# Performance work log

Measured on AMD Instinct MI355X. Metric: run time of the kernel, lower is better.

## Reference

```python
import jax, jax.numpy as jnp
import numpy as np

Nc, Nq = 100000, 20000
Fc, Fq = 300, 768
HID, H, L = 128, 4, 2
D = HID // H
OUT = 8
E = 400000
NT, ET = 2, 3


def setup_inputs() -> dict:
    key = jax.random.key(0)
    ks = jax.random.split(key, 24)
    def n(i, shape, s=1.0):
        return jax.random.normal(ks[i], shape, dtype=jnp.float32) * s
    return {
        'x_context': n(0, (Nc, Fc)),
        'x_question': n(1, (Nq, Fq)),
        'src_q2c': jax.random.randint(ks[2], (E,), 0, Nq),
        'dst_q2c': jax.random.randint(ks[3], (E,), 0, Nc),
        'src_c2c': jax.random.randint(ks[4], (E,), 0, Nc),
        'dst_c2c': jax.random.randint(ks[5], (E,), 0, Nc),
        'src_c2q': jax.random.randint(ks[6], (E,), 0, Nc),
        'dst_c2q': jax.random.randint(ks[7], (E,), 0, Nq),
        'in_W_context': n(8, (Fc, HID), 0.05),
        'in_b_context': jnp.zeros((HID,), jnp.float32),
        'in_W_question': n(9, (Fq, HID), 0.05),
        'in_b_question': jnp.zeros((HID,), jnp.float32),
        'k_W': n(10, (L, NT, HID, HID), 0.05),
        'k_b': jnp.zeros((L, NT, HID), jnp.float32),
        'q_W': n(11, (L, NT, HID, HID), 0.05),
        'q_b': jnp.zeros((L, NT, HID), jnp.float32),
        'v_W': n(12, (L, NT, HID, HID), 0.05),
        'v_b': jnp.zeros((L, NT, HID), jnp.float32),
        'a_W': n(13, (L, NT, HID, HID), 0.05),
        'a_b': jnp.zeros((L, NT, HID), jnp.float32),
        'skip': jnp.ones((L, NT), jnp.float32),
        'a_rel': n(14, (L, ET, H, D, D), 0.1),
        'm_rel': n(15, (L, ET, H, D, D), 0.1),
        'p_rel': jnp.ones((L, ET, H), jnp.float32),
        'out_W': n(16, (HID, OUT), 0.05),
        'out_b': jnp.zeros((OUT,), jnp.float32),
    }


def segment_softmax(logits, seg, num):
    # logits: [E, H], seg: [E] destination node ids
    m = jax.ops.segment_max(logits, seg, num_segments=num)
    m = jnp.where(jnp.isfinite(m), m, 0.0)
    e = jnp.exp(logits - m[seg])
    s = jax.ops.segment_sum(e, seg, num_segments=num)
    return e / (s[seg] + 1e-16)


def reference(x_context, x_question, src_q2c, dst_q2c, src_c2c, dst_c2c,
              src_c2q, dst_c2q, in_W_context, in_b_context, in_W_question,
              in_b_question, k_W, k_b, q_W, q_b, v_W, v_b, a_W, a_b, skip,
              a_rel, m_rel, p_rel, out_W, out_b):
    # node type 0 = 'context', 1 = 'question'
    x = [jax.nn.relu(x_context @ in_W_context + in_b_context),
         jax.nn.relu(x_question @ in_W_question + in_b_question)]
    Ns = [x[0].shape[0], x[1].shape[0]]
    # (src_nt, dst_nt, src_idx, dst_idx) per edge type
    edge_types = [(1, 0, src_q2c, dst_q2c),
                  (0, 0, src_c2c, dst_c2c),
                  (0, 1, src_c2q, dst_c2q)]
    scale = 1.0 / jnp.sqrt(jnp.float32(D))
    for l in range(L):
        k = [(x[nt] @ k_W[l, nt] + k_b[l, nt]).reshape(-1, H, D) for nt in range(NT)]
        q = [(x[nt] @ q_W[l, nt] + q_b[l, nt]).reshape(-1, H, D) for nt in range(NT)]
        v = [(x[nt] @ v_W[l, nt] + v_b[l, nt]).reshape(-1, H, D) for nt in range(NT)]
        agg = [jnp.zeros((Ns[nt], H, D), x[0].dtype) for nt in range(NT)]
        for et, (snt, dnt, src, dst) in enumerate(edge_types):
            k_rel = jnp.einsum('ehd,hdf->ehf', k[snt][src], a_rel[l, et])
            v_rel = jnp.einsum('ehd,hdf->ehf', v[snt][src], m_rel[l, et])
            logits = jnp.einsum('ehd,ehd->eh', q[dnt][dst], k_rel) * p_rel[l, et] * scale
            alpha = segment_softmax(logits, dst, Ns[dnt])  # [E, H]
            agg[dnt] = agg[dnt].at[dst].add(v_rel * alpha[:, :, None])
        for nt in range(NT):
            o = jax.nn.gelu(agg[nt].reshape(Ns[nt], HID), approximate=False)
            o = o @ a_W[l, nt] + a_b[l, nt]
            g = jax.nn.sigmoid(skip[l, nt])
            x[nt] = g * o + (1.0 - g) * x[nt]
    return x[0] @ out_W + out_b
```

## Files before the change

kernel.cpp:

```cpp
#include <hip/hip_runtime.h>

constexpr int NC = 100000;
constexpr int NQ = 20000;
constexpr int FC = 300;
constexpr int FQ = 768;
constexpr int NEDGE = 400000;
constexpr int NTOT = NC + NC + NQ;
constexpr int NTOT2 = NC + NQ;
constexpr int NB0 = (NC + 127) / 128;
constexpr int NB1 = (NQ + 127) / 128;
constexpr int NBALL = NB0 + NB1;
constexpr int NBC64 = (NC + 63) / 64;
constexpr int NBQ64 = (NQ + 63) / 64;
constexpr int NBALL64 = NBC64 + NBQ64;
constexpr float SCALE = 0.17677669529663687f;
constexpr float LOG2E = 1.4426950408889634f;

typedef __attribute__((ext_vector_type(8))) short bf16x8;
typedef __attribute__((ext_vector_type(4))) float f32x4;
typedef unsigned short u16;

__device__ __forceinline__ float gelu_f(float x) {
  return 0.5f * x * (1.0f + erff(x * 0.7071067811865476f));
}
__device__ __forceinline__ u16 bf16_rne(float x) {
  unsigned u = __float_as_uint(x);
  unsigned r = u + 0x7fffu + ((u >> 16) & 1u);
  return (u16)(r >> 16);
}
__device__ __forceinline__ float bf16_to_f(u16 h) {
  return __uint_as_float(((unsigned)h) << 16);
}
__device__ __forceinline__ void split2(float x, u16& hi, u16& lo) {
  hi = bf16_rne(x);
  lo = bf16_rne(x - bf16_to_f(hi));
}
__device__ __forceinline__ void splitT(float x, u16& hi, u16& lo) {
  hi = (u16)(__float_as_uint(x) >> 16);
  lo = bf16_rne(x - bf16_to_f(hi));
}

__global__ void k_count3(const int* __restrict__ d0, const int* __restrict__ d1,
                         const int* __restrict__ d2, int* __restrict__ counts) {
  int i = blockIdx.x * 256 + threadIdx.x;
  if (i >= 3 * NEDGE) return;
  int et = i / NEDGE, e = i - et * NEDGE;
  int d = (et == 0) ? d0[e] : (et == 1) ? d1[e] : d2[e];
  int base = (et == 0) ? 0 : (et == 1) ? NC : 2 * NC;
  atomicAdd(&counts[base + d], 1);
}

__global__ void k_scan_block(const int* __restrict__ in, int* __restrict__ out,
                             int* __restrict__ bsum, int n) {
  __shared__ int s[256];
  int tid = threadIdx.x;
  int i = blockIdx.x * 256 + tid;
  int v = (i < n) ? in[i] : 0;
  s[tid] = v;
  __syncthreads();
  for (int off = 1; off < 256; off <<= 1) {
    int t = (tid >= off) ? s[tid - off] : 0;
    __syncthreads();
    s[tid] += t;
    __syncthreads();
  }
  if (i < n) out[i] = s[tid] - v;
  if (tid == 255) bsum[blockIdx.x] = s[255];
}

__global__ void k_scan_sums(int* __restrict__ bsum, int nb) {
  __shared__ int s[1024];
  int tid = threadIdx.x;
  int v = (tid < nb) ? bsum[tid] : 0;
  s[tid] = v;
  __syncthreads();
  for (int off = 1; off < 1024; off <<= 1) {
    int t = (tid >= off) ? s[tid - off] : 0;
    __syncthreads();
    s[tid] += t;
    __syncthreads();
  }
  if (tid < nb) bsum[tid] = s[tid] - v;
}

__global__ void k_scan_add(int* __restrict__ ptr, const int* __restrict__ bsum,
                           int* __restrict__ cursor, int n, int total) {
  int i = blockIdx.x * 256 + threadIdx.x;
  if (i < n) {
    int v = ptr[i] + bsum[blockIdx.x];
    ptr[i] = v;
    cursor[i] = v;
  }
  if (i == 0) ptr[n] = total;
}

__global__ void k_scatter3(const int* __restrict__ s0, const int* __restrict__ s1,
                           const int* __restrict__ s2, const int* __restrict__ d0,
                           const int* __restrict__ d1, const int* __restrict__ d2,
                           int* __restrict__ cursor, int* __restrict__ srcs_out) {
  int i = blockIdx.x * 256 + threadIdx.x;
  if (i >= 3 * NEDGE) return;
  int et = i / NEDGE, e = i - et * NEDGE;
  int d = (et == 0) ? d0[e] : (et == 1) ? d1[e] : d2[e];
  int sv = (et == 0) ? s0[e] : (et == 1) ? s1[e] : s2[e];
  int base = (et == 0) ? 0 : (et == 1) ? NC : 2 * NC;
  int p = atomicAdd(&cursor[base + d], 1);
  srcs_out[p] = sv;
}

__global__ void prep_all(const float* __restrict__ kW, const float* __restrict__ kB,
                         const float* __restrict__ qW, const float* __restrict__ qB,
                         const float* __restrict__ vW, const float* __restrict__ vB,
                         const float* __restrict__ aW, const float* __restrict__ aB,
                         const float* __restrict__ arel, const float* __restrict__ mrel,
                         const float* __restrict__ prel,
                         u16* __restrict__ Bth, u16* __restrict__ Btl,
                         float* __restrict__ biasOut) {
  int i = blockIdx.x;
  int col = threadIdx.x;
  int y = blockIdx.y;
  int l = y / 10, yy = y % 10;
  size_t lw = (size_t)l * 2 * 16384, lb = (size_t)l * 2 * 128;
  size_t le = (size_t)l * 3 * 4096, lp = (size_t)l * 3 * 4;
  const float *W = nullptr, *bb = nullptr, *rel = nullptr, *pr = nullptr;
  float mscale = 1.0f;
  bool fold = false;
  switch (yy) {
    case 0: W = qW + lw; bb = qB + lb; break;
    case 1: fold = true; W = kW + lw; bb = kB + lb; rel = arel + le + 4096; pr = prel + lp + 4; mscale = SCALE; break;
    case 2: fold = true; W = vW + lw; bb = vB + lb; rel = mrel + le + 4096; break;
    case 3: fold = true; W = kW + lw; bb = kB + lb; rel = arel + le + 8192; pr = prel + lp + 8; mscale = SCALE; break;
    case 4: fold = true; W = vW + lw; bb = vB + lb; rel = mrel + le + 8192; break;
    case 5: W = qW + lw + 16384; bb = qB + lb + 128; break;
    case 6: fold = true; W = kW + lw + 16384; bb = kB + lb + 128; rel = arel + le; pr = prel + lp; mscale = SCALE; break;
    case 7: fold = true; W = vW + lw + 16384; bb = vB + lb + 128; rel = mrel + le; break;
    case 8: W = aW + lw; bb = aB + lb; break;
    default: W = aW + lw + 16384; bb = aB + lb + 128; break;
  }
  int colOff = y * 128;
  if (!fold) {
    float v = W[i * 128 + col];
    u16 hi, lo;
    split2(v, hi, lo);
    Bth[(size_t)(colOff + col) * 128 + i] = hi;
    Btl[(size_t)(colOff + col) * 128 + i] = lo;
    if (i == 0) biasOut[colOff + col] = bb[col];
    return;
  }
  int h = col >> 5, f = col & 31;
  float m = (pr ? pr[h] : 1.0f) * mscale;
  float s = 0.0f;
  #pragma unroll
  for (int d = 0; d < 32; ++d)
    s += W[i * 128 + h * 32 + d] * rel[(h * 32 + d) * 32 + f];
  s *= m;
  u16 hi, lo;
  split2(s, hi, lo);
  Bth[(size_t)(colOff + col) * 128 + i] = hi;
  Btl[(size_t)(colOff + col) * 128 + i] = lo;
  if (i == 0) {
    float sb = 0.0f;
    #pragma unroll
    for (int d = 0; d < 32; ++d)
      sb += bb[h * 32 + d] * rel[(h * 32 + d) * 32 + f];
    biasOut[colOff + col] = sb * m;
  }
}

__global__ void split_in(const float* __restrict__ Wc, const float* __restrict__ bc,
                         const float* __restrict__ Wq, const float* __restrict__ bq,
                         u16* __restrict__ Bth, u16* __restrict__ Btl,
                         float* __restrict__ biasOut) {
  int n = blockIdx.x, y = blockIdx.y;
  const float* W = y ? Wq : Wc;
  const float* b = y ? bq : bc;
  int K = y ? FQ : FC, Kp = y ? 768 : 320;
  size_t boff = y ? (size_t)128 * 320 : 0;
  for (int k = threadIdx.x; k < Kp; k += 256) {
    float v = (k < K) ? W[(size_t)k * 128 + n] : 0.0f;
    u16 hi, lo;
    split2(v, hi, lo);
    Bth[boff + (size_t)n * Kp + k] = hi;
    Btl[boff + (size_t)n * Kp + k] = lo;
  }
  if (threadIdx.x == 0) biasOut[(y ? 128 : 0) + n] = b[n];
}

template <int MODE>
__global__ __launch_bounds__(256) void pipe_gemm(
    const float* __restrict__ Ac, const float* __restrict__ Aq,
    const u16* __restrict__ Bth, const u16* __restrict__ Btl,
    const float* __restrict__ biasBuf,
    u16* __restrict__ xh_all, u16* __restrict__ xl_all,
    const float* __restrict__ skip, int l) {
  __shared__ u16 smem[15360];
  constexpr int AH = 0, AL = 2560, BH = 5120, BL = 10240;
  const int tid = threadIdx.x, lane = tid & 63, wv = tid >> 6;
  const int l15 = lane & 15, g4 = lane >> 4, koff = g4 * 8;
  const int srA = tid >> 2, scA = (tid & 3) * 8;
  const int srB = tid >> 1, scB = (tid & 1) * 16;

  const int bid = blockIdx.x;
  const int nt = (bid < NBC64) ? 0 : 1;
  const int m0 = nt ? (bid - NBC64) * 64 : bid * 64;
  const int M = nt ? NQ : NC;
  const int rowbase = nt ? NC : 0;
  const float* A32;
  int K, Kp, biasOff;
  size_t boff, arow;
  if (MODE == 1) {
    if (nt == 0) { A32 = Ac; K = FC; Kp = 320; boff = 0; biasOff = 0; }
    else { A32 = Aq; K = FQ; Kp = 768; boff = (size_t)128 * 320; biasOff = 128; }
    arow = (size_t)(m0 + srA) * K;
  } else {
    A32 = Ac;
    K = 128; Kp = 128;
    boff = (size_t)(8 + nt) * 16384;
    biasOff = (8 + nt) * 128;
    arow = (size_t)(rowbase + m0 + srA) * 128;
  }
  const bool rowokA = (m0 + srA) < M;
  const int nk = (K + 31) / 32;

  f32x4 acc[8];
  #pragma unroll
  for (int ni = 0; ni < 8; ++ni) acc[ni] = (f32x4){0.f, 0.f, 0.f, 0.f};

  auto loadA = [&](float va[8], int k0) {
    if (rowokA && (k0 + 32 <= K)) {
      const float* ap = A32 + arow + k0 + scA;
      float4 f0 = *(const float4*)ap;
      float4 f1 = *(const float4*)(ap + 4);
      va[0] = f0.x; va[1] = f0.y; va[2] = f0.z; va[3] = f0.w;
      va[4] = f1.x; va[5] = f1.y; va[6] = f1.z; va[7] = f1.w;
    } else {
      #pragma unroll
      for (int j = 0; j < 8; ++j) {
        int kc = k0 + scA + j;
        va[j] = (rowokA && kc < K) ? A32[arow + kc] : 0.0f;
      }
    }
  };
  auto loadB = [&](uint4& bh0, uint4& bh1, uint4& bl0, uint4& bl1, int k0) {
    const u16* bp = Bth + boff + (size_t)srB * Kp + k0 + scB;
    bh0 = *(const uint4*)bp;
    bh1 = *(const uint4*)(bp + 8);
    const u16* lp = Btl + boff + (size_t)srB * Kp + k0 + scB;
    bl0 = *(const uint4*)lp;
    bl1 = *(const uint4*)(lp + 8);
  };

  float vaC[8];
  uint4 bhC0, bhC1, blC0, blC1;
  loadA(vaC, 0);
  loadB(bhC0, bhC1, blC0, blC1, 0);

  for (int ks = 0; ks < nk; ++ks) {
    {
      alignas(16) u16 hv[8], lv[8];
      #pragma unroll
      for (int j = 0; j < 8; ++j) {
        float x = (MODE == 2) ? gelu_f(vaC[j]) : vaC[j];
        splitT(x, hv[j], lv[j]);
      }
      *(uint4*)&smem[AH + srA * 40 + scA] = *(const uint4*)hv;
      *(uint4*)&smem[AL + srA * 40 + scA] = *(const uint4*)lv;
      *(uint4*)&smem[BH + srB * 40 + scB] = bhC0;
      *(uint4*)&smem[BH + srB * 40 + scB + 8] = bhC1;
      *(uint4*)&smem[BL + srB * 40 + scB] = blC0;
      *(uint4*)&smem[BL + srB * 40 + scB + 8] = blC1;
    }
    __syncthreads();

    float vaN[8];
    uint4 bhN0, bhN1, blN0, blN1;
    const bool more = (ks + 1) < nk;
    if (more) {
      loadA(vaN, (ks + 1) * 32);
      loadB(bhN0, bhN1, blN0, blN1, (ks + 1) * 32);
    }

    {
      int row = wv * 16 + l15;
      bf16x8 a_h = *(const bf16x8*)&smem[AH + row * 40 + koff];
      bf16x8 a_l = *(const bf16x8*)&smem[AL + row * 40 + koff];
      #pragma unroll
      for (int ni = 0; ni < 8; ++ni) {
        int col = ni * 16 + l15;
        bf16x8 b_h = *(const bf16x8*)&smem[BH + col * 40 + koff];
        bf16x8 b_l = *(const bf16x8*)&smem[BL + col * 40 + koff];
        acc[ni] = __builtin_amdgcn_mfma_f32_16x16x32_bf16(a_h, b_h, acc[ni], 0, 0, 0);
        acc[ni] = __builtin_amdgcn_mfma_f32_16x16x32_bf16(a_l, b_h, acc[ni], 0, 0, 0);
        acc[ni] = __builtin_amdgcn_mfma_f32_16x16x32_bf16(a_h, b_l, acc[ni], 0, 0, 0);
      }
    }
    __syncthreads();

    if (more) {
      #pragma unroll
      for (int j = 0; j < 8; ++j) vaC[j] = vaN[j];
      bhC0 = bhN0; bhC1 = bhN1; blC0 = blN0; blC1 = blN1;
    }
  }

  float g = 1.0f;
  if (MODE == 2) g = 1.0f / (1.0f + __expf(-skip[l * 2 + nt]));

  const int rl0 = wv * 16 + g4 * 4;
  #pragma unroll
  for (int ni = 0; ni < 8; ++ni) {
    int colL = ni * 16 + l15;
    float bi = biasBuf[biasOff + colL];
    #pragma unroll
    for (int rr = 0; rr < 4; ++rr) {
      int row = m0 + rl0 + rr;
      float o = acc[ni][rr] + bi;
      if (MODE == 1) {
        o = fmaxf(o, 0.0f);
      } else if (row < M) {
        size_t idx = (size_t)(rowbase + row) * 128 + colL;
        float xo = bf16_to_f(xh_all[idx]) + bf16_to_f(xl_all[idx]);
        o = g * o + (1.0f - g) * xo;
      }
      acc[ni][rr] = o;
    }
  }

  const int wrow = tid >> 2, wseg = tid & 3;
  #pragma unroll
  for (int ph = 0; ph < 2; ++ph) {
    if (ph) __syncthreads();
    #pragma unroll
    for (int ni = 0; ni < 8; ++ni) {
      #pragma unroll
      for (int rr = 0; rr < 4; ++rr) {
        u16 hh, ll;
        split2(acc[ni][rr], hh, ll);
        smem[(rl0 + rr) * 136 + ni * 16 + l15] = ph ? ll : hh;
      }
    }
    __syncthreads();
    int grow = m0 + wrow;
    if (grow < M) {
      u16* dstp = ph ? xl_all : xh_all;
      uint4* dst = (uint4*)&dstp[(size_t)(rowbase + grow) * 128 + wseg * 32];
      const uint4* src = (const uint4*)&smem[wrow * 136 + wseg * 32];
      #pragma unroll
      for (int j = 0; j < 4; ++j) dst[j] = src[j];
    }
  }
}

__global__ __launch_bounds__(256) void proj_all(
    const u16* __restrict__ xh_all,
    const u16* __restrict__ Bth, const float* __restrict__ biasBuf,
    u16* __restrict__ q_all, u16* __restrict__ kvA,
    u16* __restrict__ kvB1, u16* __restrict__ kvB2, int last) {
  int bid = blockIdx.x, y = blockIdx.y;
  int nt = (bid < NB0) ? 0 : 1;
  if (nt == 1 && y >= 3) return;
  if (last) {
    if (nt == 0 && y >= 3) return;
    if (nt == 1 && y == 0) return;
  }
  __shared__ u16 smem[10240];
  constexpr int AH = 0, BH = 5120;
  int m0 = nt ? (bid - NB0) * 128 : bid * 128;
  int M = nt ? NQ : NC;
  int abase = nt ? NC : 0;
  int bslab = nt ? 5 + y : y;
  u16* cp; int ld, cb, crowbase;
  if (nt == 0) {
    switch (y) {
      case 0: cp = q_all; ld = 128; cb = 0; crowbase = 0; break;
      case 1: cp = kvB1; ld = 256; cb = 0; crowbase = 0; break;
      case 2: cp = kvB1; ld = 256; cb = 128; crowbase = 0; break;
      case 3: cp = kvB2; ld = 256; cb = 0; crowbase = 0; break;
      default: cp = kvB2; ld = 256; cb = 128; crowbase = 0; break;
    }
  } else {
    switch (y) {
      case 0: cp = q_all; ld = 128; cb = 0; crowbase = NC; break;
      case 1: cp = kvA; ld = 256; cb = 0; crowbase = 0; break;
      default: cp = kvA; ld = 256; cb = 128; crowbase = 0; break;
    }
  }
  const int tid = threadIdx.x, lane = tid & 63, wv = tid >> 6;
  const int l15 = lane & 15, g4 = lane >> 4, koff = g4 * 8;
  const int sr = tid >> 1, sc = (tid & 1) * 16;
  const bool rowok = (m0 + sr) < M;

  f32x4 acc[2][8];
  #pragma unroll
  for (int mi = 0; mi < 2; ++mi)
    #pragma unroll
    for (int ni = 0; ni < 8; ++ni) acc[mi][ni] = (f32x4){0.f, 0.f, 0.f, 0.f};

  for (int k0 = 0; k0 < 128; k0 += 32) {
    uint4 h0 = {0, 0, 0, 0}, h1 = {0, 0, 0, 0};
    if (rowok) {
      const u16* ap = xh_all + (size_t)(abase + m0 + sr) * 128 + k0 + sc;
      h0 = *(const uint4*)ap;
      h1 = *(const uint4*)(ap + 8);
    }
    *(uint4*)&smem[AH + sr * 40 + sc] = h0;
    *(uint4*)&smem[AH + sr * 40 + sc + 8] = h1;
    {
      const u16* bp = Bth + (size_t)(bslab * 128 + sr) * 128 + k0 + sc;
      *(uint4*)&smem[BH + sr * 40 + sc] = *(const uint4*)bp;
      *(uint4*)&smem[BH + sr * 40 + sc + 8] = *(const uint4*)(bp + 8);
    }
    __syncthreads();

    bf16x8 a_h[2];
    #pragma unroll
    for (int mi = 0; mi < 2; ++mi) {
      int row = wv * 32 + mi * 16 + l15;
      a_h[mi] = *(const bf16x8*)&smem[AH + row * 40 + koff];
    }
    #pragma unroll
    for (int ni = 0; ni < 8; ++ni) {
      int col = ni * 16 + l15;
      bf16x8 b_h = *(const bf16x8*)&smem[BH + col * 40 + koff];
      #pragma unroll
      for (int mi = 0; mi < 2; ++mi)
        acc[mi][ni] = __builtin_amdgcn_mfma_f32_16x16x32_bf16(a_h[mi], b_h, acc[mi][ni], 0, 0, 0);
    }
    __syncthreads();
  }

  const int wrow = tid >> 2, wseg = tid & 3;
  #pragma unroll
  for (int h = 0; h < 2; ++h) {
    if (h) __syncthreads();
    if ((wv >> 1) == h) {
      #pragma unroll
      for (int mi = 0; mi < 2; ++mi) {
        int rl = (wv & 1) * 32 + mi * 16 + g4 * 4;
        #pragma unroll
        for (int ni = 0; ni < 8; ++ni) {
          float bi = biasBuf[bslab * 128 + ni * 16 + l15];
          #pragma unroll
          for (int rr = 0; rr < 4; ++rr)
            smem[(rl + rr) * 136 + ni * 16 + l15] = bf16_rne(acc[mi][ni][rr] + bi);
        }
      }
    }
    __syncthreads();
    int grow = m0 + h * 64 + wrow;
    if (grow < M) {
      uint4* dst = (uint4*)&cp[(size_t)(crowbase + grow) * ld + cb + wseg * 32];
      const uint4* src = (const uint4*)&smem[wrow * 136 + wseg * 32];
      #pragma unroll
      for (int j = 0; j < 4; ++j) dst[j] = src[j];
    }
  }
}

__device__ __forceinline__ void attn_seg(
    const u16* __restrict__ kv, int start, int end,
    const int* __restrict__ srcs, const float q8[8], int lane, float accO[8]) {
  if (start >= end) return;
  float sum = 0.0f;
  float acc[8];
  #pragma unroll
  for (int i = 0; i < 8; ++i) acc[i] = 0.0f;
  const int half = lane >> 5;
  const int sub = lane & 31;
  const int bsrc = lane & 44;
  for (int e = start; e < end; e += 4) {
    int e0 = e + half;
    int e1 = e + 2 + half;
    bool v0 = e0 < end, v1 = e1 < end;
    int c0 = v0 ? e0 : end - 1;
    int c1 = v1 ? e1 : end - 1;
    int s0 = srcs[c0];
    int s1 = srcs[c1];
    uint4 u0 = *(const uint4*)&kv[(size_t)s0 * 256 + sub * 8];
    uint4 u1 = *(const uint4*)&kv[(size_t)s1 * 256 + sub * 8];
    float r0[8], r1[8];
    r0[0] = bf16_to_f((u16)(u0.x & 0xffffu)); r0[1] = bf16_to_f((u16)(u0.x >> 16));
    r0[2] = bf16_to_f((u16)(u0.y & 0xffffu)); r0[3] = bf16_to_f((u16)(u0.y >> 16));
    r0[4] = bf16_to_f((u16)(u0.z & 0xffffu)); r0[5] = bf16_to_f((u16)(u0.z >> 16));
    r0[6] = bf16_to_f((u16)(u0.w & 0xffffu)); r0[7] = bf16_to_f((u16)(u0.w >> 16));
    r1[0] = bf16_to_f((u16)(u1.x & 0xffffu)); r1[1] = bf16_to_f((u16)(u1.x >> 16));
    r1[2] = bf16_to_f((u16)(u1.y & 0xffffu)); r1[3] = bf16_to_f((u16)(u1.y >> 16));
    r1[4] = bf16_to_f((u16)(u1.z & 0xffffu)); r1[5] = bf16_to_f((u16)(u1.z >> 16));
    r1[6] = bf16_to_f((u16)(u1.w & 0xffffu)); r1[7] = bf16_to_f((u16)(u1.w >> 16));
    float p0 = q8[0] * r0[0];
    float p1 = q8[0] * r1[0];
    #pragma unroll
    for (int i = 1; i < 8; ++i) {
      p0 = fmaf(q8[i], r0[i], p0);
      p1 = fmaf(q8[i], r1[i], p1);
    }
    p0 += __shfl_xor(p0, 1);
    p1 += __shfl_xor(p1, 1);
    p0 += __shfl_xor(p0, 2);
    p1 += __shfl_xor(p1, 2);
    p0 = fminf(p0, 100.0f);
    p1 = fminf(p1, 100.0f);
    float w0 = v0 ? exp2f(p0) : 0.0f;
    float w1 = v1 ? exp2f(p1) : 0.0f;
    float wB0 = __shfl(w0, bsrc);
    float wB1 = __shfl(w1, bsrc);
    sum += wB0 + wB1;
    #pragma unroll
    for (int i = 0; i < 8; ++i) {
      acc[i] = fmaf(wB0, r0[i], acc[i]);
      acc[i] = fmaf(wB1, r1[i], acc[i]);
    }
  }
  sum += __shfl_xor(sum, 32);
  #pragma unroll
  for (int i = 0; i < 8; ++i) acc[i] += __shfl_xor(acc[i], 32);
  float inv = 1.0f / (sum + 1e-16f);
  #pragma unroll
  for (int i = 0; i < 8; ++i) accO[i] = fmaf(acc[i], inv, accO[i]);
}

__global__ __launch_bounds__(256) void attn_all(
    const u16* __restrict__ q_all, const u16* __restrict__ kvA,
    const u16* __restrict__ kvB1, const u16* __restrict__ kvB2,
    const int* __restrict__ ptr_all, const int* __restrict__ srcs_all,
    float* __restrict__ agg_all, int ncap) {
  int wave = threadIdx.x >> 6, lane = threadIdx.x & 63;
  int node = blockIdx.x * 4 + wave;
  if (node >= ncap) return;
  int sub = lane & 31;
  float q8[8];
  #pragma unroll
  for (int i = 0; i < 8; ++i) q8[i] = 0.0f;
  if (sub < 16) {
    uint4 u = *(const uint4*)&q_all[(size_t)node * 128 + sub * 8];
    q8[0] = bf16_to_f((u16)(u.x & 0xffffu)) * LOG2E; q8[1] = bf16_to_f((u16)(u.x >> 16)) * LOG2E;
    q8[2] = bf16_to_f((u16)(u.y & 0xffffu)) * LOG2E; q8[3] = bf16_to_f((u16)(u.y >> 16)) * LOG2E;
    q8[4] = bf16_to_f((u16)(u.z & 0xffffu)) * LOG2E; q8[5] = bf16_to_f((u16)(u.z >> 16)) * LOG2E;
    q8[6] = bf16_to_f((u16)(u.w & 0xffffu)) * LOG2E; q8[7] = bf16_to_f((u16)(u.w >> 16)) * LOG2E;
  }
  float accO[8];
  #pragma unroll
  for (int i = 0; i < 8; ++i) accO[i] = 0.0f;
  if (node < NC) {
    attn_seg(kvA, ptr_all[node], ptr_all[node + 1], srcs_all, q8, lane, accO);
    attn_seg(kvB1, ptr_all[NC + node], ptr_all[NC + node + 1], srcs_all, q8, lane, accO);
  } else {
    int idx = 2 * NC + (node - NC);
    attn_seg(kvB2, ptr_all[idx], ptr_all[idx + 1], srcs_all, q8, lane, accO);
  }
  if (lane >= 16 && lane < 32) {
    int j = lane - 16;
    float4 o0 = {accO[0], accO[1], accO[2], accO[3]};
    float4 o1 = {accO[4], accO[5], accO[6], accO[7]};
    *(float4*)&agg_all[(size_t)node * 128 + j * 8] = o0;
    *(float4*)&agg_all[(size_t)node * 128 + j * 8 + 4] = o1;
  }
}

__global__ __launch_bounds__(256) void gemm_out(const u16* __restrict__ Xh,
                                                const u16* __restrict__ Xl,
                                                const float* __restrict__ W,
                                                const float* __restrict__ b,
                                                float* __restrict__ out, int M) {
  __shared__ float Ws[1024];
  __shared__ float As[32][129];
  int tid = threadIdx.x;
  int m0 = blockIdx.x * 32;
  *(float4*)&Ws[tid * 4] = *(const float4*)&W[tid * 4];
  {
    int r = tid >> 3;
    int c0 = (tid & 7) * 16;
    if (m0 + r < M) {
      const u16* hp = Xh + (size_t)(m0 + r) * 128 + c0;
      const u16* lp = Xl + (size_t)(m0 + r) * 128 + c0;
      #pragma unroll
      for (int j = 0; j < 16; ++j) As[r][c0 + j] = bf16_to_f(hp[j]) + bf16_to_f(lp[j]);
    } else {
      #pragma unroll
      for (int j = 0; j < 16; ++j) As[r][c0 + j] = 0.0f;
    }
  }
  __syncthreads();
  int r = tid >> 3, c = tid & 7;
  float sum = b[c];
  #pragma unroll 16
  for (int k = 0; k < 128; ++k) sum = fmaf(As[r][k], Ws[k * 8 + c], sum);
  if (m0 + r < M) out[(size_t)(m0 + r) * 8 + c] = sum;
}

static inline size_t align256(size_t x) { return (x + 255) & ~(size_t)255; }

extern "C" void kernel_launch(void* const* d_in, const int* in_sizes, int n_in,
                              void* d_out, int out_size, void* d_ws, size_t ws_size,
                              hipStream_t stream) {
  const float* x_context = (const float*)d_in[0];
  const float* x_question = (const float*)d_in[1];
  const int* src_q2c = (const int*)d_in[2];
  const int* dst_q2c = (const int*)d_in[3];
  const int* src_c2c = (const int*)d_in[4];
  const int* dst_c2c = (const int*)d_in[5];
  const int* src_c2q = (const int*)d_in[6];
  const int* dst_c2q = (const int*)d_in[7];
  const float* inWc = (const float*)d_in[8];
  const float* inbc = (const float*)d_in[9];
  const float* inWq = (const float*)d_in[10];
  const float* inbq = (const float*)d_in[11];
  const float* kW = (const float*)d_in[12];
  const float* kB = (const float*)d_in[13];
  const float* qW = (const float*)d_in[14];
  const float* qB = (const float*)d_in[15];
  const float* vW = (const float*)d_in[16];
  const float* vB = (const float*)d_in[17];
  const float* aW = (const float*)d_in[18];
  const float* aB = (const float*)d_in[19];
  const float* skip = (const float*)d_in[20];
  const float* arel = (const float*)d_in[21];
  const float* mrel = (const float*)d_in[22];
  const float* prel = (const float*)d_in[23];
  const float* outW = (const float*)d_in[24];
  const float* outb = (const float*)d_in[25];

  char* base = (char*)d_ws;
  size_t off = 0;
  auto carve = [&](size_t bytes) -> void* {
    void* p = base + off;
    off = align256(off + bytes);
    return p;
  };
  u16* xh_all = (u16*)carve((size_t)NTOT2 * 128 * 2);
  u16* xl_all = (u16*)carve((size_t)NTOT2 * 128 * 2);
  u16* q_all = (u16*)carve((size_t)NTOT2 * 128 * 2);
  u16* kvA = (u16*)carve((size_t)NQ * 256 * 2);
  u16* kvB1 = (u16*)carve((size_t)NC * 256 * 2);
  u16* kvB2 = (u16*)carve((size_t)NC * 256 * 2);
  float* agg_all = (float*)carve((size_t)NTOT2 * 128 * 4);
  u16* Bth = (u16*)carve((size_t)2560 * 128 * 2);
  u16* Btl = (u16*)carve((size_t)2560 * 128 * 2);
  u16* BthI = (u16*)carve((size_t)(320 + 768) * 128 * 2);
  u16* BtlI = (u16*)carve((size_t)(320 + 768) * 128 * 2);
  float* biasBuf = (float*)carve(2560 * 4);
  float* biasIn = (float*)carve(256 * 4);
  int* ptr_all = (int*)carve((size_t)(NTOT + 1) * 4);
  int* srcs_all = (int*)carve((size_t)3 * NEDGE * 4);
  int* counts = (int*)carve((size_t)NTOT * 4);
  int* cursor = (int*)carve((size_t)NTOT * 4);
  int* blksums = (int*)carve(2048 * 4);

  {
    int nb = (NTOT + 255) / 256;
    hipMemsetAsync(counts, 0, (size_t)NTOT * 4, stream);
    k_count3<<<(3 * NEDGE + 255) / 256, 256, 0, stream>>>(dst_q2c, dst_c2c, dst_c2q, counts);
    k_scan_block<<<nb, 256, 0, stream>>>(counts, ptr_all, blksums, NTOT);
    k_scan_sums<<<1, 1024, 0, stream>>>(blksums, nb);
    k_scan_add<<<nb, 256, 0, stream>>>(ptr_all, blksums, cursor, NTOT, 3 * NEDGE);
    k_scatter3<<<(3 * NEDGE + 255) / 256, 256, 0, stream>>>(
        src_q2c, src_c2c, src_c2q, dst_q2c, dst_c2c, dst_c2q, cursor, srcs_all);
  }

  split_in<<<dim3(128, 2), 256, 0, stream>>>(inWc, inbc, inWq, inbq, BthI, BtlI, biasIn);
  prep_all<<<dim3(128, 20), 128, 0, stream>>>(kW, kB, qW, qB, vW, vB, aW, aB,
                                              arel, mrel, prel, Bth, Btl, biasBuf);

  pipe_gemm<1><<<NBALL64, 256, 0, stream>>>(x_context, x_question, BthI, BtlI, biasIn,
                                            xh_all, xl_all, nullptr, 0);

  for (int l = 0; l < 2; ++l) {
    const int last = (l == 1);
    const u16* BthL = Bth + (size_t)l * 10 * 128 * 128;
    const u16* BtlL = Btl + (size_t)l * 10 * 128 * 128;
    const float* biasL = biasBuf + (size_t)l * 1280;
    proj_all<<<dim3(NBALL, 5), 256, 0, stream>>>(xh_all, BthL, biasL,
                                                 q_all, kvA, kvB1, kvB2, last);
    int ncap = last ? NC : NTOT2;
    attn_all<<<(ncap + 3) / 4, 256, 0, stream>>>(q_all, kvA, kvB1, kvB2,
                                                 ptr_all, srcs_all, agg_all, ncap);
    pipe_gemm<2><<<last ? NBC64 : NBALL64, 256, 0, stream>>>(agg_all, nullptr, BthL, BtlL, biasL,
                                                             xh_all, xl_all, skip, l);
  }

  gemm_out<<<(NC + 31) / 32, 256, 0, stream>>>(xh_all, xl_all, outW, outb, (float*)d_out, NC);
}
```

Measured before the change: 696.2 us.

## Use 128-row tiles in input and output GEMMs, drop prefetch and A-low split for GELU path

The input-projection and post-attention GEMMs now use 128-row tiles with two M sub-tiles per wave instead of 64-row tiles, so each B fragment loaded from LDS feeds twice as many MFMAs. The register prefetch of the next K slice is removed, leaving a plain load-sync-compute loop. In the GELU (MODE 2) path the activation is rounded to a single bf16 instead of a hi/lo pair, which drops one of the three MFMAs per fragment at some precision cost. The epilogue writes out the 128-row tile in two halves through shared memory.

```diff
diff --git a/kernel.cpp b/kernel.cpp
--- a/kernel.cpp
+++ b/kernel.cpp
@@ -10,9 +10,6 @@
 constexpr int NB0 = (NC + 127) / 128;
 constexpr int NB1 = (NQ + 127) / 128;
 constexpr int NBALL = NB0 + NB1;
-constexpr int NBC64 = (NC + 63) / 64;
-constexpr int NBQ64 = (NQ + 63) / 64;
-constexpr int NBALL64 = NBC64 + NBQ64;
 constexpr float SCALE = 0.17677669529663687f;
 constexpr float LOG2E = 1.4426950408889634f;
 
@@ -187,22 +184,25 @@
 }
 
 template <int MODE>
-__global__ __launch_bounds__(256) void pipe_gemm(
+__global__ __launch_bounds__(256) void big_gemm(
     const float* __restrict__ Ac, const float* __restrict__ Aq,
     const u16* __restrict__ Bth, const u16* __restrict__ Btl,
     const float* __restrict__ biasBuf,
     u16* __restrict__ xh_all, u16* __restrict__ xl_all,
     const float* __restrict__ skip, int l) {
-  __shared__ u16 smem[15360];
-  constexpr int AH = 0, AL = 2560, BH = 5120, BL = 10240;
+  constexpr int NS = (MODE == 1) ? 20480 : 15360;
+  constexpr int AHo = 0;
+  constexpr int ALo = 5120;
+  constexpr int BHo = (MODE == 1) ? 10240 : 5120;
+  constexpr int BLo = BHo + 5120;
+  __shared__ u16 smem[NS];
   const int tid = threadIdx.x, lane = tid & 63, wv = tid >> 6;
   const int l15 = lane & 15, g4 = lane >> 4, koff = g4 * 8;
-  const int srA = tid >> 2, scA = (tid & 3) * 8;
-  const int srB = tid >> 1, scB = (tid & 1) * 16;
+  const int sr = tid >> 1, sc16 = (tid & 1) * 16;
 
   const int bid = blockIdx.x;
-  const int nt = (bid < NBC64) ? 0 : 1;
-  const int m0 = nt ? (bid - NBC64) * 64 : bid * 64;
+  const int nt = (bid < NB0) ? 0 : 1;
+  const int m0 = nt ? (bid - NB0) * 128 : bid * 128;
   const int M = nt ? NQ : NC;
   const int rowbase = nt ? NC : 0;
   const float* A32;
@@ -211,142 +211,141 @@
   if (MODE == 1) {
     if (nt == 0) { A32 = Ac; K = FC; Kp = 320; boff = 0; biasOff = 0; }
     else { A32 = Aq; K = FQ; Kp = 768; boff = (size_t)128 * 320; biasOff = 128; }
-    arow = (size_t)(m0 + srA) * K;
+    arow = (size_t)(m0 + sr) * K;
   } else {
     A32 = Ac;
     K = 128; Kp = 128;
     boff = (size_t)(8 + nt) * 16384;
     biasOff = (8 + nt) * 128;
-    arow = (size_t)(rowbase + m0 + srA) * 128;
-  }
-  const bool rowokA = (m0 + srA) < M;
-  const int nk = (K + 31) / 32;
-
-  f32x4 acc[8];
-  #pragma unroll
-  for (int ni = 0; ni < 8; ++ni) acc[ni] = (f32x4){0.f, 0.f, 0.f, 0.f};
-
-  auto loadA = [&](float va[8], int k0) {
+    arow = (size_t)(rowbase + m0 + sr) * 128;
+  }
+  const bool rowokA = (m0 + sr) < M;
+
+  f32x4 acc[2][8];
+  #pragma unroll
+  for (int mi = 0; mi < 2; ++mi)
+    #pragma unroll
+    for (int ni = 0; ni < 8; ++ni) acc[mi][ni] = (f32x4){0.f, 0.f, 0.f, 0.f};
+
+  for (int k0 = 0; k0 < K; k0 += 32) {
+    float va[16];
     if (rowokA && (k0 + 32 <= K)) {
-      const float* ap = A32 + arow + k0 + scA;
-      float4 f0 = *(const float4*)ap;
-      float4 f1 = *(const float4*)(ap + 4);
-      va[0] = f0.x; va[1] = f0.y; va[2] = f0.z; va[3] = f0.w;
-      va[4] = f1.x; va[5] = f1.y; va[6] = f1.z; va[7] = f1.w;
+      const float* ap = A32 + arow + k0 + sc16;
+      #pragma unroll
+      for (int j = 0; j < 4; ++j) {
+        float4 f = *(const float4*)(ap + 4 * j);
+        va[4 * j + 0] = f.x; va[4 * j + 1] = f.y; va[4 * j + 2] = f.z; va[4 * j + 3] = f.w;
+      }
     } else {
       #pragma unroll
-      for (int j = 0; j < 8; ++j) {
-        int kc = k0 + scA + j;
+      for (int j = 0; j < 16; ++j) {
+        int kc = k0 + sc16 + j;
         va[j] = (rowokA && kc < K) ? A32[arow + kc] : 0.0f;
       }
     }
-  };
-  auto loadB = [&](uint4& bh0, uint4& bh1, uint4& bl0, uint4& bl1, int k0) {
-    const u16* bp = Bth + boff + (size_t)srB * Kp + k0 + scB;
-    bh0 = *(const uint4*)bp;
-    bh1 = *(const uint4*)(bp + 8);
-    const u16* lp = Btl + boff + (size_t)srB * Kp + k0 + scB;
-    bl0 = *(const uint4*)lp;
-    bl1 = *(const uint4*)(lp + 8);
-  };
-
-  float vaC[8];
-  uint4 bhC0, bhC1, blC0, blC1;
-  loadA(vaC, 0);
-  loadB(bhC0, bhC1, blC0, blC1, 0);
-
-  for (int ks = 0; ks < nk; ++ks) {
+    if (MODE == 1) {
+      alignas(16) u16 hv[16], lv[16];
+      #pragma unroll
+      for (int j = 0; j < 16; ++j) splitT(va[j], hv[j], lv[j]);
+      *(uint4*)&smem[AHo + sr * 40 + sc16] = *(const uint4*)&hv[0];
+      *(uint4*)&smem[AHo + sr * 40 + sc16 + 8] = *(const uint4*)&hv[8];
+      *(uint4*)&smem[ALo + sr * 40 + sc16] = *(const uint4*)&lv[0];
+      *(uint4*)&smem[ALo + sr * 40 + sc16 + 8] = *(const uint4*)&lv[8];
+    } else {
+      alignas(16) u16 hv[16];
+      #pragma unroll
+      for (int j = 0; j < 16; ++j) hv[j] = bf16_rne(gelu_f(va[j]));
+      *(uint4*)&smem[AHo + sr * 40 + sc16] = *(const uint4*)&hv[0];
+      *(uint4*)&smem[AHo + sr * 40 + sc16 + 8] = *(const uint4*)&hv[8];
+    }
     {
-      alignas(16) u16 hv[8], lv[8];
-      #pragma unroll
-      for (int j = 0; j < 8; ++j) {
-        float x = (MODE == 2) ? gelu_f(vaC[j]) : vaC[j];
-        splitT(x, hv[j], lv[j]);
+      const u16* bp = Bth + boff + (size_t)sr * Kp + k0 + sc16;
+      *(uint4*)&smem[BHo + sr * 40 + sc16] = *(const uint4*)bp;
+      *(uint4*)&smem[BHo + sr * 40 + sc16 + 8] = *(const uint4*)(bp + 8);
+      const u16* lp = Btl + boff + (size_t)sr * Kp + k0 + sc16;
+      *(uint4*)&smem[BLo + sr * 40 + sc16] = *(const uint4*)lp;
+      *(uint4*)&smem[BLo + sr * 40 + sc16 + 8] = *(const uint4*)(lp + 8);
+    }
+    __syncthreads();
+
+    bf16x8 a_h[2], a_l[2];
+    #pragma unroll
+    for (int mi = 0; mi < 2; ++mi) {
+      int row = wv * 32 + mi * 16 + l15;
+      a_h[mi] = *(const bf16x8*)&smem[AHo + row * 40 + koff];
+      if (MODE == 1) a_l[mi] = *(const bf16x8*)&smem[ALo + row * 40 + koff];
+    }
+    #pragma unroll
+    for (int ni = 0; ni < 8; ++ni) {
+      int col = ni * 16 + l15;
+      bf16x8 b_h = *(const bf16x8*)&smem[BHo + col * 40 + koff];
+      bf16x8 b_l = *(const bf16x8*)&smem[BLo + col * 40 + koff];
+      #pragma unroll
+      for (int mi = 0; mi < 2; ++mi) {
+        acc[mi][ni] = __builtin_amdgcn_mfma_f32_16x16x32_bf16(a_h[mi], b_h, acc[mi][ni], 0, 0, 0);
+        if (MODE == 1)
+          acc[mi][ni] = __builtin_amdgcn_mfma_f32_16x16x32_bf16(a_l[mi], b_h, acc[mi][ni], 0, 0, 0);
+        acc[mi][ni] = __builtin_amdgcn_mfma_f32_16x16x32_bf16(a_h[mi], b_l, acc[mi][ni], 0, 0, 0);
       }
-      *(uint4*)&smem[AH + srA * 40 + scA] = *(const uint4*)hv;
-      *(uint4*)&smem[AL + srA * 40 + scA] = *(const uint4*)lv;
-      *(uint4*)&smem[BH + srB * 40 + scB] = bhC0;
-      *(uint4*)&smem[BH + srB * 40 + scB + 8] = bhC1;
-      *(uint4*)&smem[BL + srB * 40 + scB] = blC0;
-      *(uint4*)&smem[BL + srB * 40 + scB + 8] = blC1;
-    }
-    __syncthreads();
-
-    float vaN[8];
-    uint4 bhN0, bhN1, blN0, blN1;
-    const bool more = (ks + 1) < nk;
-    if (more) {
-      loadA(vaN, (ks + 1) * 32);
-      loadB(bhN0, bhN1, blN0, blN1, (ks + 1) * 32);
-    }
-
-    {
-      int row = wv * 16 + l15;
-      bf16x8 a_h = *(const bf16x8*)&smem[AH + row * 40 + koff];
-      bf16x8 a_l = *(const bf16x8*)&smem[AL + row * 40 + koff];
-      #pragma unroll
-      for (int ni = 0; ni < 8; ++ni) {
-        int col = ni * 16 + l15;
-        bf16x8 b_h = *(const bf16x8*)&smem[BH + col * 40 + koff];
-        bf16x8 b_l = *(const bf16x8*)&smem[BL + col * 40 + koff];
-        acc[ni] = __builtin_amdgcn_mfma_f32_16x16x32_bf16(a_h, b_h, acc[ni], 0, 0, 0);
-        acc[ni] = __builtin_amdgcn_mfma_f32_16x16x32_bf16(a_l, b_h, acc[ni], 0, 0, 0);
-        acc[ni] = __builtin_amdgcn_mfma_f32_16x16x32_bf16(a_h, b_l, acc[ni], 0, 0, 0);
-      }
-    }
-    __syncthreads();
-
-    if (more) {
-      #pragma unroll
-      for (int j = 0; j < 8; ++j) vaC[j] = vaN[j];
-      bhC0 = bhN0; bhC1 = bhN1; blC0 = blN0; blC1 = blN1;
-    }
+    }
+    __syncthreads();
   }
 
   float g = 1.0f;
   if (MODE == 2) g = 1.0f / (1.0f + __expf(-skip[l * 2 + nt]));
 
-  const int rl0 = wv * 16 + g4 * 4;
-  #pragma unroll
-  for (int ni = 0; ni < 8; ++ni) {
-    int colL = ni * 16 + l15;
-    float bi = biasBuf[biasOff + colL];
-    #pragma unroll
-    for (int rr = 0; rr < 4; ++rr) {
-      int row = m0 + rl0 + rr;
-      float o = acc[ni][rr] + bi;
-      if (MODE == 1) {
-        o = fmaxf(o, 0.0f);
-      } else if (row < M) {
-        size_t idx = (size_t)(rowbase + row) * 128 + colL;
-        float xo = bf16_to_f(xh_all[idx]) + bf16_to_f(xl_all[idx]);
-        o = g * o + (1.0f - g) * xo;
+  #pragma unroll
+  for (int mi = 0; mi < 2; ++mi) {
+    #pragma unroll
+    for (int ni = 0; ni < 8; ++ni) {
+      int colL = ni * 16 + l15;
+      float bi = biasBuf[biasOff + colL];
+      #pragma unroll
+      for (int rr = 0; rr < 4; ++rr) {
+        int row = m0 + wv * 32 + mi * 16 + g4 * 4 + rr;
+        float o = acc[mi][ni][rr] + bi;
+        if (MODE == 1) {
+          o = fmaxf(o, 0.0f);
+        } else if (row < M) {
+          size_t idx = (size_t)(rowbase + row) * 128 + colL;
+          float xo = bf16_to_f(xh_all[idx]) + bf16_to_f(xl_all[idx]);
+          o = g * o + (1.0f - g) * xo;
+        }
+        acc[mi][ni][rr] = o;
       }
-      acc[ni][rr] = o;
     }
   }
 
   const int wrow = tid >> 2, wseg = tid & 3;
   #pragma unroll
   for (int ph = 0; ph < 2; ++ph) {
-    if (ph) __syncthreads();
-    #pragma unroll
-    for (int ni = 0; ni < 8; ++ni) {
-      #pragma unroll
-      for (int rr = 0; rr < 4; ++rr) {
-        u16 hh, ll;
-        split2(acc[ni][rr], hh, ll);
-        smem[(rl0 + rr) * 136 + ni * 16 + l15] = ph ? ll : hh;
+    #pragma unroll
+    for (int h = 0; h < 2; ++h) {
+      if (ph || h) __syncthreads();
+      if ((wv >> 1) == h) {
+        #pragma unroll
+        for (int mi = 0; mi < 2; ++mi) {
+          int rl = (wv & 1) * 32 + mi * 16 + g4 * 4;
+          #pragma unroll
+          for (int ni = 0; ni < 8; ++ni) {
+            #pragma unroll
+            for (int rr = 0; rr < 4; ++rr) {
+              u16 hh, ll;
+              split2(acc[mi][ni][rr], hh, ll);
+              smem[(rl + rr) * 136 + ni * 16 + l15] = ph ? ll : hh;
+            }
+          }
+        }
       }
-    }
-    __syncthreads();
-    int grow = m0 + wrow;
-    if (grow < M) {
-      u16* dstp = ph ? xl_all : xh_all;
-      uint4* dst = (uint4*)&dstp[(size_t)(rowbase + grow) * 128 + wseg * 32];
-      const uint4* src = (const uint4*)&smem[wrow * 136 + wseg * 32];
-      #pragma unroll
-      for (int j = 0; j < 4; ++j) dst[j] = src[j];
+      __syncthreads();
+      int grow = m0 + h * 64 + wrow;
+      if (grow < M) {
+        u16* dstp = ph ? xl_all : xh_all;
+        uint4* dst = (uint4*)&dstp[(size_t)(rowbase + grow) * 128 + wseg * 32];
+        const uint4* src = (const uint4*)&smem[wrow * 136 + wseg * 32];
+        #pragma unroll
+        for (int j = 0; j < 4; ++j) dst[j] = src[j];
+      }
     }
   }
 }
@@ -661,8 +660,8 @@
   prep_all<<<dim3(128, 20), 128, 0, stream>>>(kW, kB, qW, qB, vW, vB, aW, aB,
                                               arel, mrel, prel, Bth, Btl, biasBuf);
 
-  pipe_gemm<1><<<NBALL64, 256, 0, stream>>>(x_context, x_question, BthI, BtlI, biasIn,
-                                            xh_all, xl_all, nullptr, 0);
+  big_gemm<1><<<NBALL, 256, 0, stream>>>(x_context, x_question, BthI, BtlI, biasIn,
+                                         xh_all, xl_all, nullptr, 0);
 
   for (int l = 0; l < 2; ++l) {
     const int last = (l == 1);
@@ -674,8 +673,8 @@
     int ncap = last ? NC : NTOT2;
     attn_all<<<(ncap + 3) / 4, 256, 0, stream>>>(q_all, kvA, kvB1, kvB2,
                                                  ptr_all, srcs_all, agg_all, ncap);
-    pipe_gemm<2><<<last ? NBC64 : NBALL64, 256, 0, stream>>>(agg_all, nullptr, BthL, BtlL, biasL,
-                                                             xh_all, xl_all, skip, l);
+    big_gemm<2><<<last ? NB0 : NBALL, 256, 0, stream>>>(agg_all, nullptr, BthL, BtlL, biasL,
+                                                        xh_all, xl_all, skip, l);
   }
 
   gemm_out<<<(NC + 31) / 32, 256, 0, stream>>>(xh_all, xl_all, outW, outb, (float*)d_out, NC);
```

Measured after the change: 728.9 us. +4.7%, slower.
